# Performance work log

Measured on AMD Instinct MI355X. Metric: run time of the kernel, lower is better.

The kernel has to match this reference:

```python
import jax, jax.numpy as jnp
import numpy as np

HEAD = 32  # HEAD_SIZE
B, T, C = 8, 1024, 768
LAYER_ID, N_LAYER = 2, 12


def wkv7(r, w, k, v, a, b):
    # RWKV7 linear recurrence (matches the custom CUDA 'attn' kernel math):
    #   S = S * exp(-exp(w)) + (S @ a) b^T + v k^T ;  y = S @ r
    Bb, Tt, Cc = r.shape
    H, N = Cc // HEAD, HEAD
    rs = lambda z: jnp.moveaxis(z.reshape(Bb, Tt, H, N), 1, 0)  # [T,B,H,N]
    rT, kT, vT, aT, bT = rs(r), rs(k), rs(v), rs(a), rs(b)
    wT = rs(jnp.exp(-jnp.exp(w)))  # decay in (0,1)
    def step(S, inp):
        rt, wt, kt, vt, at, bt = inp  # each [B,H,N]
        sa = jnp.einsum('bhij,bhj->bhi', S, at)
        S = S * wt[:, :, None, :] + sa[..., None] * bt[:, :, None, :] + vt[..., None] * kt[:, :, None, :]
        return S, jnp.einsum('bhij,bhj->bhi', S, rt)
    S0 = jnp.zeros((Bb, H, N, N), r.dtype)
    _, y = jax.lax.scan(step, S0, (rT, wT, kT, vT, aT, bT))
    return jnp.moveaxis(y, 0, 1).reshape(Bb, Tt, Cc)


def setup_inputs() -> dict:
    key = jax.random.key(0)
    ks = iter(jax.random.split(key, 64))
    def rn(shape, s=0.02):
        return (jax.random.normal(next(ks), shape, jnp.float32) * s)
    def un(shape, lim):
        return jax.random.uniform(next(ks), shape, jnp.float32, -lim, lim)
    H, N = C // HEAD, HEAD
    r10 = 1.0 - LAYER_ID / N_LAYER          # ratio_1_to_almost0
    r01 = LAYER_ID / (N_LAYER - 1)          # ratio_0_to_1
    ddd = (np.arange(C, dtype=np.float64) / C).reshape(1, 1, C)
    f32 = lambda z: jnp.asarray(z, jnp.float32)
    time_maa_x = f32(1.0 - ddd ** (0.6 * r10 ** 0.9))
    time_maa_rg = f32(1.0 - ddd ** (0.2 * r10))
    time_maa_wa = f32(1.0 - ddd ** (0.9 * r10))
    time_maa_k = f32(1.0 - (ddd ** (0.9 * r10) + 0.4 * r01))
    time_maa_v = f32(1.0 - (ddd ** (0.4 * r10) + 0.6 * r01))
    ds = -7.0 + 5.0 * (np.arange(C, dtype=np.float64) / (C - 1)) ** (0.85 + r01 ** 0.5)
    time_decay = f32(ds.reshape(1, 1, C) + 0.5)
    inp = {
        'x': jax.random.normal(next(ks), (B, T, C), jnp.float32),
        'v1': jax.random.normal(next(ks), (B, T, C), jnp.float32),
        'time_maa_x': time_maa_x, 'time_maa_rg': time_maa_rg, 'time_maa_wa': time_maa_wa,
        'time_maa_k': time_maa_k, 'time_maa_v': time_maa_v,
        'time_decay': time_decay,
        'time_faaaa': rn((1, 1, H, N), 0.05),
        'time_aaaaa': rn((1, 1, C), 0.05),
        'time_maa_w1': rn((C, 28 * 4)), 'time_maa_w2': rn((4, 28, C), 0.05),
        'time_decay_w1': rn((C, 64)), 'time_decay_w2': rn((64, C), 0.05),
        'time_aaa_w1': rn((C, 24)), 'time_aaa_w2': rn((24, C), 0.05),
        'time_kkk_w1': rn((C, 24)), 'time_kkk_w2': rn((24, C), 0.05),
        'gate_w1': rn((C, 120)), 'gate_w2': rn((120, C), 0.05),
        'ma_w1': rn((C, 24)), 'ma_w2': rn((24, C), 0.05), 'time_misc_a': rn((1, 1, C), 0.05),
        'mk_w1': rn((C, 24)), 'mk_w2': rn((24, C), 0.05), 'time_misc_k': rn((1, 1, C), 0.05),
        'mv_w1': rn((C, 24)), 'mv_w2': rn((24, C), 0.05), 'time_misc_v': 1.0 + rn((1, 1, C), 0.05),
        'Wr': un((C, C), 0.5 / C ** 0.5), 'Wk': un((C, C), 0.05 / C ** 0.5),
        'Wv': un((C, C), 0.5 / C ** 0.5), 'Wo': rn((C, C), 0.02),
        'ln_w': jnp.ones((C,), jnp.float32), 'ln_b': jnp.zeros((C,), jnp.float32),
    }
    return inp


def reference(x, v1, time_maa_x, time_maa_rg, time_maa_wa, time_maa_k, time_maa_v,
              time_decay, time_faaaa, time_aaaaa, time_maa_w1, time_maa_w2,
              time_decay_w1, time_decay_w2, time_aaa_w1, time_aaa_w2,
              time_kkk_w1, time_kkk_w2, gate_w1, gate_w2, ma_w1, ma_w2, time_misc_a,
              mk_w1, mk_w2, time_misc_k, mv_w1, mv_w2, time_misc_v,
              Wr, Wk, Wv, Wo, ln_w, ln_b):
    Bb, Tt, Cc = x.shape
    H, N = Cc // HEAD, HEAD
    # token shift: xx[t] = x[t-1] - x[t], with x[-1] = 0
    xsh = jnp.concatenate([jnp.zeros_like(x[:, :1]), x[:, :-1]], axis=1)
    xx = xsh - x
    xxx = x + xx * time_maa_x
    tm = jnp.tanh(xxx @ time_maa_w1).reshape(Bb, Tt, 4, -1)      # [B,T,4,28]
    mix = jnp.einsum('btfd,fdc->fbtc', tm, time_maa_w2)          # [4,B,T,C]
    xrg = x + xx * (time_maa_rg + mix[0])
    xwa = x + xx * (time_maa_wa + mix[1])
    xk = x + xx * (time_maa_k + mix[2])
    xv = x + xx * (time_maa_v + mix[3])
    r = xrg @ Wr
    w = -jax.nn.softplus(-(time_decay + jnp.tanh(xwa @ time_decay_w1) @ time_decay_w2)) - 0.5
    k = xk @ Wk
    v = xv @ Wv
    v = v + (v1 - v) * jax.nn.sigmoid(time_misc_v + xv @ mv_w1 @ mv_w2)
    g = jax.nn.sigmoid(xrg @ gate_w1) @ gate_w2
    kk = k + jnp.tanh(xk @ time_kkk_w1) @ time_kkk_w2
    kk4 = kk.reshape(Bb, Tt, H, N)
    nrm = jnp.maximum(jnp.sqrt(jnp.sum(kk4 * kk4, axis=-1, keepdims=True)), 1e-12)
    kk = (kk4 / nrm).reshape(Bb, Tt, Cc)
    a = jax.nn.sigmoid(time_aaaaa + xwa @ time_aaa_w1 @ time_aaa_w2)
    ma = jax.nn.sigmoid(time_misc_a + xwa @ ma_w1 @ ma_w2)
    k = k * ma + k * a * (1.0 - ma)
    mk = jax.nn.sigmoid(time_misc_k + xk @ mk_w1 @ mk_w2)
    k = k * jnp.exp(jnp.minimum(w * mk, 0.0))
    y = wkv7(r, w, k, v, -kk, kk * a)
    # GroupNorm(n_head groups) over each token, eps=6.4e-5
    yg = y.reshape(Bb, Tt, H, N)
    mu = jnp.mean(yg, axis=-1, keepdims=True)
    var = jnp.var(yg, axis=-1, keepdims=True)
    yn = (yg - mu) * jax.lax.rsqrt(var + 6.4e-05)
    yn = yn * ln_w.reshape(H, N) + ln_b.reshape(H, N)
    # per-head bonus term
    bonus = (jnp.sum(r.reshape(Bb, Tt, H, N) * k.reshape(Bb, Tt, H, N) * time_faaaa,
                     axis=-1, keepdims=True) * v.reshape(Bb, Tt, H, N))
    y = yn.reshape(Bb, Tt, Cc) + bonus.reshape(Bb, Tt, Cc)
    out = (y * g) @ Wo
    return (out, v1)
```

## Files before the change

kernel.cpp:

```cpp
#include <hip/hip_runtime.h>
#include <hip/hip_bf16.h>
#include <math.h>

#define Bdim 8
#define Tdim 1024
#define Cdim 768
#define Hdim 24
#define Ndim 32
#define BTdim (Bdim*Tdim)

typedef __attribute__((ext_vector_type(8))) short bf16x8;
typedef __attribute__((ext_vector_type(4))) float f32x4;
typedef __hip_bfloat16 bf16;

__device__ __forceinline__ float sigm(float x){ return 1.f/(1.f+expf(-x)); }
__device__ __forceinline__ float softplusf(float x){ return fmaxf(x,0.f) + log1pf(expf(-fabsf(x))); }
__device__ __forceinline__ float bf2f(bf16 v){ return __bfloat162float(v); }
__device__ __forceinline__ float us2f(unsigned short s){ return __builtin_bit_cast(float, (unsigned)s<<16); }

template<int CTRL>
__device__ __forceinline__ float dpp_add(float x){
  int xi = __builtin_bit_cast(int, x);
  int yi = __builtin_amdgcn_mov_dpp(xi, CTRL, 0xF, 0xF, true);
  return x + __builtin_bit_cast(float, yi);
}
__device__ __forceinline__ float red32(float x){
  x = dpp_add<0xB1>(x);
  x = dpp_add<0x4E>(x);
  x = dpp_add<0x141>(x);
  x = dpp_add<0x140>(x);
  x += __shfl_xor(x, 16);
  return x;
}
__device__ __forceinline__ float red16(float x){
  x = dpp_add<0xB1>(x);
  x = dpp_add<0x4E>(x);
  x = dpp_add<0x141>(x);
  x = dpp_add<0x140>(x);
  return x;
}

#define GLDS16(gp, lp) __builtin_amdgcn_global_load_lds((const __attribute__((address_space(1))) void*)(gp), (__attribute__((address_space(3))) void*)(lp), 16, 0, 0)

__global__ void k1_shift(const float* __restrict__ x, const float* __restrict__ maa_x,
                         bf16* __restrict__ xxx) {
  int idx = blockIdx.x*256 + threadIdx.x;
  if (idx >= BTdim*Cdim) return;
  int c = idx % Cdim; int row = idx / Cdim; int t = row % Tdim;
  float xv = x[idx];
  float xp = (t==0) ? 0.f : x[idx - Cdim];
  xxx[idx] = __float2bfloat16(xv + (xp - xv)*maa_x[c]);
}

__global__ __launch_bounds__(256) void kcp(const float* __restrict__ W0, const float* __restrict__ W1,
    const float* __restrict__ W2, const float* __restrict__ W3,
    bf16* __restrict__ T0, bf16* __restrict__ T1, bf16* __restrict__ T2, bf16* __restrict__ T3,
    const float* __restrict__ dw1, const float* __restrict__ aaa_w1,
    const float* __restrict__ ma_w1, const float* __restrict__ kkk_w1, const float* __restrict__ mk_w1,
    const float* __restrict__ mv_w1, const float* __restrict__ gate_w1, const float* __restrict__ maa_w1,
    const float* __restrict__ dw2, const float* __restrict__ aaa_w2, const float* __restrict__ ma_w2,
    const float* __restrict__ kkk_w2, const float* __restrict__ mk_w2, const float* __restrict__ mv_w2,
    const float* __restrict__ gate_w2,
    bf16* __restrict__ PWwa, bf16* __restrict__ PWk, bf16* __restrict__ PWv,
    bf16* __restrict__ PWrg, bf16* __restrict__ PWmaa,
    bf16* __restrict__ W2wa, bf16* __restrict__ W2k, bf16* __restrict__ W2v, bf16* __restrict__ W2g){
  const int bid = blockIdx.x;
  if (bid < 2304) {
    __shared__ float tile[32][33];
    const int z = bid/576, rem = bid - z*576;
    const int by = (rem/24)*32, bx = (rem%24)*32;
    const float* Wsrc[4] = {W0,W1,W2,W3};
    bf16* Tdst[4] = {T0,T1,T2,T3};
    const float* W = Wsrc[z];
    bf16* T = Tdst[z];
    int tx = threadIdx.x & 31, ty = threadIdx.x >> 5;
    #pragma unroll
    for (int q=0;q<32;q+=8) tile[ty+q][tx] = W[(size_t)(by+ty+q)*Cdim + bx+tx];
    __syncthreads();
    #pragma unroll
    for (int q=0;q<32;q+=8) T[(size_t)(bx+ty+q)*Cdim + by+tx] = __float2bfloat16(tile[tx][ty+q]);
    return;
  }
  int idx = (bid-2304)*256 + threadIdx.x;
  if (idx < 491520) {
    int buf = idx / 98304, rem = idx - buf*98304;
    int n = rem / 768, kk = rem - n*768;
    float val = 0.f;
    bf16* dst;
    switch(buf){
      case 0: dst=PWwa; if(n<64) val=dw1[(size_t)kk*64+n]; else if(n<88) val=aaa_w1[(size_t)kk*24+(n-64)]; else if(n<112) val=ma_w1[(size_t)kk*24+(n-88)]; break;
      case 1: dst=PWk;  if(n<24) val=kkk_w1[(size_t)kk*24+n]; else if(n<48) val=mk_w1[(size_t)kk*24+(n-24)]; break;
      case 2: dst=PWv;  if(n<24) val=mv_w1[(size_t)kk*24+n]; break;
      case 3: dst=PWrg; if(n<120) val=gate_w1[(size_t)kk*120+n]; break;
      default: dst=PWmaa; if(n<112) val=maa_w1[(size_t)kk*112+n]; break;
    }
    dst[rem] = __float2bfloat16(val);
    return;
  }
  int i = idx - 491520;
  if (i < 294912){
    int n=i>>7, q=i&127, seg=n/768, c=n-seg*768;
    float val=0.f;
    if (seg==0){ if(q<64) val=dw2[(size_t)q*768+c]; }
    else if (seg==1){ if(q>=64&&q<88) val=aaa_w2[(size_t)(q-64)*768+c]; }
    else { if(q>=88&&q<112) val=ma_w2[(size_t)(q-88)*768+c]; }
    W2wa[i]=__float2bfloat16(val); return;
  }
  i -= 294912;
  if (i < 98304){
    int n=i>>6, q=i&63, seg=n/768, c=n-seg*768;
    float val=0.f;
    if (seg==0){ if(q<24) val=kkk_w2[(size_t)q*768+c]; }
    else { if(q>=24&&q<48) val=mk_w2[(size_t)(q-24)*768+c]; }
    W2k[i]=__float2bfloat16(val); return;
  }
  i -= 98304;
  if (i < 24576){
    int c=i>>5, q=i&31;
    float val = (q<24) ? mv_w2[(size_t)q*768+c] : 0.f;
    W2v[i]=__float2bfloat16(val); return;
  }
  i -= 24576;
  if (i < 98304){
    int c=i>>7, q=i&127;
    float val = (q<120) ? gate_w2[(size_t)q*768+c] : 0.f;
    W2g[i]=__float2bfloat16(val);
  }
}

__global__ __launch_bounds__(256) void gemm_wo(const bf16* __restrict__ A,
    const bf16* __restrict__ Bt, float* __restrict__ C, int N, int K) {
  const int bid = blockIdx.x;
  const int bm = (bid & 127)*64, bn = (bid >> 7)*128;
  __shared__ unsigned short As[64*32];
  __shared__ unsigned short Bs[128*32];
  const int tid = threadIdx.x, lane = tid&63, w = tid>>6;
  const int wr = w>>1, wc = w&1;
  const int lr = lane&15, kg = lane>>4;
  f32x4 zero = {0.f,0.f,0.f,0.f};
  f32x4 acc[2][4];
  #pragma unroll
  for (int m=0;m<2;m++)
    #pragma unroll
    for (int n=0;n<4;n++) acc[m][n]=zero;
  const size_t rowA = (size_t)(bm + w*16 + (lane>>2))*K + (lane&3)*8;
  const size_t rowB = (size_t)(bn + w*32 + (lane>>2))*K + (lane&3)*8;
  unsigned short* lA = As + w*16*32;
  unsigned short* lB = Bs + w*32*32;
  for (int k0=0; k0<K; k0+=32){
    GLDS16(A + rowA + k0,                 lA);
    GLDS16(Bt + rowB + k0,                lB);
    GLDS16(Bt + rowB + k0 + (size_t)16*K, lB + 512);
    __syncthreads();
    bf16x8 af[2], bfr[4];
    #pragma unroll
    for (int m=0;m<2;m++) af[m]  = *(const bf16x8*)(void*)(As + (wr*32+m*16+lr)*32 + kg*8);
    #pragma unroll
    for (int n=0;n<4;n++) bfr[n] = *(const bf16x8*)(void*)(Bs + (wc*64+n*16+lr)*32 + kg*8);
    #pragma unroll
    for (int m=0;m<2;m++)
      #pragma unroll
      for (int n=0;n<4;n++)
        acc[m][n] = __builtin_amdgcn_mfma_f32_16x16x32_bf16(af[m], bfr[n], acc[m][n], 0,0,0);
    __syncthreads();
  }
  #pragma unroll
  for (int m=0;m<2;m++)
    #pragma unroll
    for (int n=0;n<4;n++){
      size_t r0 = (size_t)(bm + wr*32 + m*16 + kg*4);
      int cc = bn + wc*64 + n*16 + lr;
      #pragma unroll
      for (int q=0;q<4;q++)
        C[(r0+q)*N + cc] = acc[m][n][q];
    }
}

__global__ __launch_bounds__(256) void gemm_tm(const bf16* __restrict__ A,
    const bf16* __restrict__ Bt, float* __restrict__ C, int K) {
  const int bm = blockIdx.x*64;
  __shared__ unsigned short As[64*32];
  __shared__ unsigned short Bs[128*32];
  const int tid = threadIdx.x, lane = tid&63, w = tid>>6;
  const int wr = w>>1, wc = w&1;
  const int lr = lane&15, kg = lane>>4;
  f32x4 zero = {0.f,0.f,0.f,0.f};
  f32x4 acc[2][4];
  #pragma unroll
  for (int m=0;m<2;m++)
    #pragma unroll
    for (int n=0;n<4;n++) acc[m][n]=zero;
  const size_t rowA = (size_t)(bm + w*16 + (lane>>2))*K + (lane&3)*8;
  const size_t rowB = (size_t)(w*32 + (lane>>2))*K + (lane&3)*8;
  unsigned short* lA = As + w*16*32;
  unsigned short* lB = Bs + w*32*32;
  for (int k0=0; k0<K; k0+=32){
    GLDS16(A + rowA + k0,                 lA);
    GLDS16(Bt + rowB + k0,                lB);
    GLDS16(Bt + rowB + k0 + (size_t)16*K, lB + 512);
    __syncthreads();
    bf16x8 af[2], bfr[4];
    #pragma unroll
    for (int m=0;m<2;m++) af[m]  = *(const bf16x8*)(void*)(As + (wr*32+m*16+lr)*32 + kg*8);
    #pragma unroll
    for (int n=0;n<4;n++) bfr[n] = *(const bf16x8*)(void*)(Bs + (wc*64+n*16+lr)*32 + kg*8);
    #pragma unroll
    for (int m=0;m<2;m++)
      #pragma unroll
      for (int n=0;n<4;n++)
        acc[m][n] = __builtin_amdgcn_mfma_f32_16x16x32_bf16(af[m], bfr[n], acc[m][n], 0,0,0);
    __syncthreads();
  }
  #pragma unroll
  for (int m=0;m<2;m++)
    #pragma unroll
    for (int n=0;n<4;n++){
      size_t r0 = (size_t)(bm + wr*32 + m*16 + kg*4);
      int cc = wc*64 + n*16 + lr;
      if (cc < 112){
        #pragma unroll
        for (int q=0;q<4;q++)
          C[(r0+q)*112 + cc] = tanhf(acc[m][n][q]);
      }
    }
}

struct S1P {
  const bf16* A[4];
  const bf16* Bt[4];
  bf16* C[4];
  int Ntrue[4];
  int Nalloc[4];
  int act[4];
};
struct G3 {
  const bf16* A[3];
  const bf16* Bt[3];
  bf16* C[3];
};
__global__ __launch_bounds__(256) void gemm_s1b3(S1P s, G3 g, int K) {
  const int bid = blockIdx.x;
  __shared__ unsigned short As[128*32];
  __shared__ unsigned short Bs[128*32];
  const int tid = threadIdx.x, lane = tid&63, w = tid>>6;
  const int wr = w>>1, wc = w&1;
  const int lr = lane&15, kg = lane>>4;
  int bm, bn, z;
  const bf16 *A, *Bt;
  const bool small = (bid < 256);
  if (small){
    z = bid>>6; bm = (bid&63)*128; bn = 0;
    A = s.A[z]; Bt = s.Bt[z];
  } else {
    int rem = bid-256;
    bn = (rem/192)*128; int t2 = rem%192;
    z = t2/64; bm = (t2%64)*128;
    A = g.A[z]; Bt = g.Bt[z];
  }
  f32x4 zero = {0.f,0.f,0.f,0.f};
  f32x4 acc[4][4];
  #pragma unroll
  for (int m=0;m<4;m++)
    #pragma unroll
    for (int n=0;n<4;n++) acc[m][n]=zero;
  const size_t rowA = (size_t)(bm + w*32 + (lane>>2))*K + (lane&3)*8;
  const size_t rowB = (size_t)(bn + w*32 + (lane>>2))*K + (lane&3)*8;
  unsigned short* lA = As + w*32*32;
  unsigned short* lB = Bs + w*32*32;
  for (int k0=0; k0<K; k0+=32){
    GLDS16(A + rowA + k0,                 lA);
    GLDS16(A + rowA + k0 + (size_t)16*K,  lA + 512);
    GLDS16(Bt + rowB + k0,                lB);
    GLDS16(Bt + rowB + k0 + (size_t)16*K, lB + 512);
    __syncthreads();
    bf16x8 af[4], bfr[4];
    #pragma unroll
    for (int m=0;m<4;m++) af[m]  = *(const bf16x8*)(void*)(As + (wr*64+m*16+lr)*32 + kg*8);
    #pragma unroll
    for (int n=0;n<4;n++) bfr[n] = *(const bf16x8*)(void*)(Bs + (wc*64+n*16+lr)*32 + kg*8);
    #pragma unroll
    for (int m=0;m<4;m++)
      #pragma unroll
      for (int n=0;n<4;n++)
        acc[m][n] = __builtin_amdgcn_mfma_f32_16x16x32_bf16(af[m], bfr[n], acc[m][n], 0,0,0);
    __syncthreads();
  }
  if (small){
    bf16* __restrict__ C = s.C[z];
    const int Ntrue = s.Ntrue[z], Nalloc = s.Nalloc[z], act = s.act[z];
    #pragma unroll
    for (int m=0;m<4;m++)
      #pragma unroll
      for (int n=0;n<4;n++){
        size_t r0 = (size_t)(bm + wr*64 + m*16 + kg*4);
        int cc = wc*64 + n*16 + lr;
        if (cc < Nalloc){
          #pragma unroll
          for (int q=0;q<4;q++){
            float val = acc[m][n][q];
            if      (act==1){ if (cc<64) val = tanhf(val); }
            else if (act==2){ if (cc<24) val = tanhf(val); }
            else if (act==3){ val = sigm(val); }
            if (cc >= Ntrue) val = 0.f;
            C[(r0+q)*Nalloc + cc] = __float2bfloat16(val);
          }
        }
      }
  } else {
    bf16* __restrict__ C = g.C[z];
    #pragma unroll
    for (int m=0;m<4;m++)
      #pragma unroll
      for (int n=0;n<4;n++){
        size_t r0 = (size_t)(bm + wr*64 + m*16 + kg*4);
        int cc = bn + wc*64 + n*16 + lr;
        #pragma unroll
        for (int q=0;q<4;q++)
          C[(r0+q)*Cdim + cc] = __float2bfloat16(acc[m][n][q]);
      }
  }
}

struct Z4 {
  const bf16* A[4];
  const bf16* Bt[4];
  bf16* C[4];
  int N[4];
  int K[4];
};
__global__ __launch_bounds__(256) void gemm_z(Z4 p) {
  const int bid = blockIdx.x;
  const int qs = bid >> 6;
  const int bm = (bid & 63) * 128;
  int z, bnq;
  if (qs < 18){ z=0; bnq=qs; }
  else if (qs < 30){ z=1; bnq=qs-18; }
  else if (qs < 36){ z=2; bnq=qs-30; }
  else { z=3; bnq=qs-36; }
  const int bn = bnq*128;
  const int N = p.N[z], K = p.K[z];
  const bf16* __restrict__ A  = p.A[z];
  const bf16* __restrict__ Bt = p.Bt[z];
  bf16* __restrict__ C = p.C[z];
  __shared__ unsigned short As[128*32];
  __shared__ unsigned short Bs[128*32];
  const int tid = threadIdx.x, lane = tid&63, w = tid>>6;
  const int wr = w>>1, wc = w&1;
  const int lr = lane&15, kg = lane>>4;
  f32x4 zero = {0.f,0.f,0.f,0.f};
  f32x4 acc[4][4];
  #pragma unroll
  for (int m=0;m<4;m++)
    #pragma unroll
    for (int n=0;n<4;n++) acc[m][n]=zero;
  const size_t rowA = (size_t)(bm + w*32 + (lane>>2))*K + (lane&3)*8;
  const size_t rowB = (size_t)(bn + w*32 + (lane>>2))*K + (lane&3)*8;
  unsigned short* lA = As + w*32*32;
  unsigned short* lB = Bs + w*32*32;
  for (int k0=0; k0<K; k0+=32){
    GLDS16(A + rowA + k0,                 lA);
    GLDS16(A + rowA + k0 + (size_t)16*K,  lA + 512);
    GLDS16(Bt + rowB + k0,                lB);
    GLDS16(Bt + rowB + k0 + (size_t)16*K, lB + 512);
    __syncthreads();
    bf16x8 af[4], bfr[4];
    #pragma unroll
    for (int m=0;m<4;m++) af[m]  = *(const bf16x8*)(void*)(As + (wr*64+m*16+lr)*32 + kg*8);
    #pragma unroll
    for (int n=0;n<4;n++) bfr[n] = *(const bf16x8*)(void*)(Bs + (wc*64+n*16+lr)*32 + kg*8);
    #pragma unroll
    for (int m=0;m<4;m++)
      #pragma unroll
      for (int n=0;n<4;n++)
        acc[m][n] = __builtin_amdgcn_mfma_f32_16x16x32_bf16(af[m], bfr[n], acc[m][n], 0,0,0);
    __syncthreads();
  }
  #pragma unroll
  for (int m=0;m<4;m++)
    #pragma unroll
    for (int n=0;n<4;n++){
      size_t r0 = (size_t)(bm + wr*64 + m*16 + kg*4);
      int cc = bn + wc*64 + n*16 + lr;
      #pragma unroll
      for (int q=0;q<4;q++)
        C[(r0+q)*N + cc] = __float2bfloat16(acc[m][n][q]);
    }
}

__global__ __launch_bounds__(256) void k2_mix(const float* __restrict__ x,
    const float* __restrict__ tm, const float* __restrict__ w2,
    const float* __restrict__ mrg, const float* __restrict__ mwa,
    const float* __restrict__ mk_, const float* __restrict__ mv_,
    bf16* __restrict__ xrg, bf16* __restrict__ xwa, bf16* __restrict__ xk, bf16* __restrict__ xv) {
  const int row0 = blockIdx.x*8, tid = threadIdx.x;
  __shared__ float stm[8][112];
  for (int idx=tid; idx<8*112; idx+=256){
    int rr=idx/112, q=idx-rr*112;
    stm[rr][q]=tm[(size_t)(row0+rr)*112+q];
  }
  __syncthreads();
  for (int c=tid;c<Cdim;c+=256){
    float x8[8], d8[8];
    #pragma unroll
    for (int rr=0;rr<8;rr++){
      size_t i=(size_t)(row0+rr)*Cdim+c;
      float xv = x[i];
      float xp = (((row0+rr) & (Tdim-1)) == 0) ? 0.f : x[i - Cdim];
      x8[rr]=xv; d8[rr]=xp - xv;
    }
    float mrgc=mrg[c], mwac=mwa[c], mkc=mk_[c], mvc=mv_[c];
    float m0[8]={},m1[8]={},m2[8]={},m3[8]={};
    #pragma unroll 4
    for (int d=0; d<28; d++){
      float w0=w2[(size_t)(d)*Cdim + c];
      float w1=w2[(size_t)(28+d)*Cdim + c];
      float w2v=w2[(size_t)(56+d)*Cdim + c];
      float w3=w2[(size_t)(84+d)*Cdim + c];
      #pragma unroll
      for (int rr=0;rr<8;rr++){
        m0[rr]+=stm[rr][d]*w0; m1[rr]+=stm[rr][28+d]*w1;
        m2[rr]+=stm[rr][56+d]*w2v; m3[rr]+=stm[rr][84+d]*w3;
      }
    }
    #pragma unroll
    for (int rr=0;rr<8;rr++){
      size_t i=(size_t)(row0+rr)*Cdim+c;
      xrg[i]=__float2bfloat16(x8[rr] + d8[rr]*(mrgc+m0[rr]));
      xwa[i]=__float2bfloat16(x8[rr] + d8[rr]*(mwac+m1[rr]));
      xk[i] =__float2bfloat16(x8[rr] + d8[rr]*(mkc+m2[rr]));
      xv[i] =__float2bfloat16(x8[rr] + d8[rr]*(mvc+m3[rr]));
    }
  }
}

__global__ __launch_bounds__(256) void k5_fuse(
    const bf16* __restrict__ zwa, const bf16* __restrict__ zk, const bf16* __restrict__ zv,
    const bf16* __restrict__ rbf, const bf16* __restrict__ kbf, bf16* __restrict__ vbf,
    const float* __restrict__ td, const float* __restrict__ aaaaa,
    const float* __restrict__ misc_a, const float* __restrict__ misc_k, const float* __restrict__ misc_v,
    const float* __restrict__ v1,
    float* __restrict__ wexp, unsigned short* __restrict__ rkab) {
  const int row = blockIdx.x, tid = threadIdx.x;
  #pragma unroll
  for (int it=0;it<3;it++){
    const int c = tid + it*256;
    const size_t i = (size_t)row*Cdim + c;
    float kraw = bf2f(kbf[i]);
    float v0   = bf2f(vbf[i]);
    float zd = bf2f(zwa[(size_t)row*2304 + c]);
    float za = bf2f(zwa[(size_t)row*2304 + 768 + c]);
    float zma= bf2f(zwa[(size_t)row*2304 + 1536 + c]);
    float zkk= bf2f(zk[(size_t)row*1536 + c]);
    float zmk= bf2f(zk[(size_t)row*1536 + 768 + c]);
    float zmv= bf2f(zv[i]);
    float w = -softplusf(-(td[c]+zd)) - 0.5f;
    wexp[i] = expf(-expf(w));
    float a  = sigm(aaaaa[c]+za);
    float ma = sigm(misc_a[c]+zma);
    float mk = sigm(misc_k[c]+zmk);
    float mv = sigm(misc_v[c]+zmv);
    vbf[i] = __float2bfloat16(v0 + (v1[i]-v0)*mv);
    float kf = kraw*(ma + a*(1.f-ma))*expf(fminf(w*mk,0.f));
    float kk = kraw + zkk;
    float ss = red32(kk*kk);
    float kkn = kk * (1.f/fmaxf(sqrtf(ss),1e-12f));
    unsigned rus = (unsigned)__builtin_bit_cast(unsigned short, rbf[i]);
    unsigned kus = (unsigned)__builtin_bit_cast(unsigned short, __float2bfloat16(kf));
    unsigned aus = (unsigned)__builtin_bit_cast(unsigned short, __float2bfloat16(-kkn));
    unsigned bus = (unsigned)__builtin_bit_cast(unsigned short, __float2bfloat16(kkn*a));
    uint2 pk;
    pk.x = rus | (kus<<16);
    pk.y = aus | (bus<<16);
    *(uint2*)&rkab[((size_t)row*Hdim + (c>>5))*128 + (size_t)(c&31)*4] = pk;
  }
}

__global__ __launch_bounds__(64) void k6_wkv(const unsigned short* __restrict__ rkab,
    const float* __restrict__ wd, const unsigned short* __restrict__ vbf, bf16* __restrict__ y) {
  const int lane = threadIdx.x;
  const int bid = blockIdx.x;
  const int head = bid % (Bdim*Hdim);
  const int rq   = bid / (Bdim*Hdim);
  const int bb = head / Hdim, hh = head - bb*Hdim;
  const int i0 = rq*4 + (lane >> 4);
  const int jh = lane & 15;
  __shared__ __align__(16) unsigned short srk[2][16][128];
  __shared__ __align__(16) float sw[2][16][32];
  __shared__ __align__(16) unsigned short sv[2][16][32];
  const size_t wvbase = (size_t)bb*Tdim*Cdim + (size_t)hh*Ndim;
  float S0=0.f, S1=0.f;

  auto rkrow = [&](size_t t){ return (((size_t)bb*Tdim + t)*Hdim + hh)*128; };
  auto STAGE = [&](int c, int buf){
    const size_t tb = (size_t)c*16;
    #pragma unroll
    for (int i=0;i<4;i++)
      GLDS16(rkab + rkrow(tb + i*4 + (lane>>4)) + (size_t)(lane&15)*8, &srk[buf][i*4][0]);
    GLDS16(wd + wvbase + (tb +     (lane>>3))*Cdim + (lane&7)*4, &sw[buf][0][0]);
    GLDS16(wd + wvbase + (tb + 8 + (lane>>3))*Cdim + (lane&7)*4, &sw[buf][8][0]);
    GLDS16(vbf + wvbase + (tb + (lane>>2))*Cdim + (lane&3)*8, &sv[buf][0][0]);
  };

  uint4 nq; float2 nw; unsigned short nv;
  auto LOADT = [&](int buf, int t){
    nq = *(const uint4*)&srk[buf][t][jh*8];
    nw = *(const float2*)&sw[buf][t][jh*2];
    nv = sv[buf][t][i0];
  };

  STAGE(0, 0);
  asm volatile("s_waitcnt vmcnt(0)" ::: "memory");
  LOADT(0, 0);
  int buf = 0;
  const int NCH = Tdim/16;
  for (int c=0; c<NCH; ++c){
    if (c+1 < NCH) STAGE(c+1, buf^1);
    const size_t yb = wvbase + (size_t)c*16*Cdim;
    #pragma unroll
    for (int t=0; t<16; t++){
      const uint4 q = nq;
      const float2 cw = nw;
      const unsigned short cv = nv;
      if (t < 15) {
        LOADT(buf, t+1);
      } else if (c+1 < NCH) {
        asm volatile("s_waitcnt vmcnt(0)" ::: "memory");
        LOADT(buf^1, 0);
      }
      float r0 = __builtin_bit_cast(float, q.x<<16);
      float k0 = __builtin_bit_cast(float, q.x & 0xFFFF0000u);
      float a0 = __builtin_bit_cast(float, q.y<<16);
      float b0 = __builtin_bit_cast(float, q.y & 0xFFFF0000u);
      float r1 = __builtin_bit_cast(float, q.z<<16);
      float k1 = __builtin_bit_cast(float, q.z & 0xFFFF0000u);
      float a1 = __builtin_bit_cast(float, q.w<<16);
      float b1 = __builtin_bit_cast(float, q.w & 0xFFFF0000u);
      const float vl = us2f(cv);
      float sa = S0*a0 + S1*a1;
      sa = red16(sa);
      S0 = S0*cw.x + (sa*b0 + vl*k0);
      S1 = S1*cw.y + (sa*b1 + vl*k1);
      float yv = S0*r0 + S1*r1;
      yv = red16(yv);
      if (jh == 0) y[yb + (size_t)t*Cdim + i0] = __float2bfloat16(yv);
    }
    buf ^= 1;
  }
}

__global__ __launch_bounds__(256) void k7_post(const bf16* __restrict__ y,
    const unsigned short* __restrict__ rkab, const bf16* __restrict__ v,
    const bf16* __restrict__ g, const float* __restrict__ faaaa,
    const float* __restrict__ lnw, const float* __restrict__ lnb,
    bf16* __restrict__ ygate,
    const float4* __restrict__ v1c, float4* __restrict__ outc) {
  const int row = blockIdx.x, tid = threadIdx.x;
  if (tid < 192) outc[(size_t)row*192 + tid] = v1c[(size_t)row*192 + tid];
  #pragma unroll
  for (int it=0; it<3; it++){
    const int c = tid + it*256;
    const size_t i = (size_t)row*Cdim + c;
    float yv = bf2f(y[i]);
    unsigned rk = *(const unsigned*)&rkab[((size_t)row*Hdim + (c>>5))*128 + (size_t)(c&31)*4];
    float rf = __builtin_bit_cast(float, rk<<16);
    float kf = __builtin_bit_cast(float, rk & 0xFFFF0000u);
    float bon = rf*kf*faaaa[c];
    float s  = red32(yv);
    float ss = red32(yv*yv);
    float bn = red32(bon);
    float mu = s*(1.f/Ndim);
    float var = ss*(1.f/Ndim) - mu*mu;
    float rs = rsqrtf(var + 6.4e-5f);
    float yn = (yv-mu)*rs*lnw[c]+lnb[c];
    ygate[i]=__float2bfloat16((yn + bn*bf2f(v[i]))*bf2f(g[i]));
  }
}

extern "C" void kernel_launch(void* const* d_in, const int* in_sizes, int n_in,
                              void* d_out, int out_size, void* d_ws, size_t ws_size,
                              hipStream_t stream) {
  const float* x      = (const float*)d_in[0];
  const float* v1     = (const float*)d_in[1];
  const float* maa_x  = (const float*)d_in[2];
  const float* maa_rg = (const float*)d_in[3];
  const float* maa_wa = (const float*)d_in[4];
  const float* maa_k  = (const float*)d_in[5];
  const float* maa_v  = (const float*)d_in[6];
  const float* time_decay = (const float*)d_in[7];
  const float* faaaa  = (const float*)d_in[8];
  const float* aaaaa  = (const float*)d_in[9];
  const float* maa_w1 = (const float*)d_in[10];
  const float* maa_w2 = (const float*)d_in[11];
  const float* dw1    = (const float*)d_in[12];
  const float* dw2    = (const float*)d_in[13];
  const float* aaa_w1 = (const float*)d_in[14];
  const float* aaa_w2 = (const float*)d_in[15];
  const float* kkk_w1 = (const float*)d_in[16];
  const float* kkk_w2 = (const float*)d_in[17];
  const float* gate_w1= (const float*)d_in[18];
  const float* gate_w2= (const float*)d_in[19];
  const float* ma_w1  = (const float*)d_in[20];
  const float* ma_w2  = (const float*)d_in[21];
  const float* misc_a = (const float*)d_in[22];
  const float* mk_w1  = (const float*)d_in[23];
  const float* mk_w2  = (const float*)d_in[24];
  const float* misc_k = (const float*)d_in[25];
  const float* mv_w1  = (const float*)d_in[26];
  const float* mv_w2  = (const float*)d_in[27];
  const float* misc_v = (const float*)d_in[28];
  const float* Wr     = (const float*)d_in[29];
  const float* Wk     = (const float*)d_in[30];
  const float* Wv     = (const float*)d_in[31];
  const float* Wo     = (const float*)d_in[32];
  const float* lnw    = (const float*)d_in[33];
  const float* lnb    = (const float*)d_in[34];
  float* out = (float*)d_out;

  float* ws = (float*)d_ws;
  const size_t BTC = (size_t)BTdim*Cdim;
  const size_t HB  = BTC/2;
  float* wexp  = ws;
  bf16* kb_bf  = (bf16*)(ws + 2*HB);
  bf16* ybuf_bf= (bf16*)(ws + 2*HB);
  bf16* vb_bf  = (bf16*)(ws + 3*HB);
  bf16* xrg_bf = (bf16*)(ws + 4*HB);
  bf16* xwa_bf = xrg_bf + BTC;
  bf16* zwa_bf = (bf16*)(ws + 4*HB);
  bf16* xk_bf  = (bf16*)(ws + 7*HB);
  bf16* xv_bf  = xk_bf + BTC;
  bf16* zk_bf  = (bf16*)(ws + 7*HB);
  bf16* xxx_bf = (bf16*)(ws + 9*HB);
  bf16* zv_bf  = (bf16*)(ws + 9*HB);
  float* tm    = ws + 10*HB;
  bf16* zg_bf  = (bf16*)(ws + 10*HB);
  bf16* hwa_bf = (bf16*)(ws + 11*HB);
  bf16* hk_bf  = hwa_bf + (size_t)BTdim*128;
  bf16* hv_bf  = hk_bf  + (size_t)BTdim*64;
  bf16* hrg_bf = hv_bf  + (size_t)BTdim*32;
  unsigned short* rkab = (unsigned short*)(ws + 12*HB);
  bf16* rb_bf  = (bf16*)(ws + 16*HB);
  bf16* yg_bf  = (bf16*)(ws + 17*HB);
  bf16* Wbase  = (bf16*)(ws + 18*HB);
  bf16* WtR = Wbase;
  bf16* WtK = WtR + 589824;
  bf16* WtV = WtK + 589824;
  bf16* WtO = WtV + 589824;
  bf16* PWwa = WtO + 589824;
  bf16* PWk  = PWwa + 98304;
  bf16* PWv  = PWk  + 98304;
  bf16* PWrg = PWv  + 98304;
  bf16* PWmaa= PWrg + 98304;
  bf16* W2wa = PWmaa + 98304;
  bf16* W2k  = W2wa + 294912;
  bf16* W2v  = W2k  + 98304;
  bf16* W2g  = W2v  + 24576;

  dim3 blk(256);
  k1_shift<<<dim3((BTdim*Cdim+255)/256), blk, 0, stream>>>(x, maa_x, xxx_bf);
  kcp<<<dim3(2304+3936), blk, 0, stream>>>(Wr,Wk,Wv,Wo, WtR,WtK,WtV,WtO,
                                           dw1,aaa_w1,ma_w1,kkk_w1,mk_w1,mv_w1,gate_w1,maa_w1,
                                           dw2,aaa_w2,ma_w2,kkk_w2,mk_w2,mv_w2,gate_w2,
                                           PWwa,PWk,PWv,PWrg,PWmaa, W2wa,W2k,W2v,W2g);
  gemm_tm<<<dim3(128), blk, 0, stream>>>(xxx_bf, PWmaa, tm, Cdim);
  k2_mix<<<dim3(BTdim/8), blk, 0, stream>>>(x, tm, maa_w2, maa_rg, maa_wa, maa_k, maa_v,
                                            xrg_bf, xwa_bf, xk_bf, xv_bf);
  {
    S1P s{};
    s.A[0]=xwa_bf; s.Bt[0]=PWwa; s.C[0]=hwa_bf; s.Ntrue[0]=112; s.Nalloc[0]=128; s.act[0]=1;
    s.A[1]=xk_bf;  s.Bt[1]=PWk;  s.C[1]=hk_bf;  s.Ntrue[1]=48;  s.Nalloc[1]=64;  s.act[1]=2;
    s.A[2]=xv_bf;  s.Bt[2]=PWv;  s.C[2]=hv_bf;  s.Ntrue[2]=24;  s.Nalloc[2]=32;  s.act[2]=0;
    s.A[3]=xrg_bf; s.Bt[3]=PWrg; s.C[3]=hrg_bf; s.Ntrue[3]=120; s.Nalloc[3]=128; s.act[3]=3;
    G3 g{};
    g.A[0]=xrg_bf; g.Bt[0]=WtR; g.C[0]=rb_bf;
    g.A[1]=xk_bf;  g.Bt[1]=WtK; g.C[1]=kb_bf;
    g.A[2]=xv_bf;  g.Bt[2]=WtV; g.C[2]=vb_bf;
    gemm_s1b3<<<dim3(256 + 3*384), blk, 0, stream>>>(s, g, Cdim);
  }
  {
    Z4 p{};
    p.A[0]=hwa_bf; p.Bt[0]=W2wa; p.C[0]=zwa_bf; p.N[0]=2304; p.K[0]=128;
    p.A[1]=hk_bf;  p.Bt[1]=W2k;  p.C[1]=zk_bf;  p.N[1]=1536; p.K[1]=64;
    p.A[2]=hv_bf;  p.Bt[2]=W2v;  p.C[2]=zv_bf;  p.N[2]=768;  p.K[2]=32;
    p.A[3]=hrg_bf; p.Bt[3]=W2g;  p.C[3]=zg_bf;  p.N[3]=768;  p.K[3]=128;
    gemm_z<<<dim3(42*64), blk, 0, stream>>>(p);
  }
  k5_fuse<<<dim3(BTdim), blk, 0, stream>>>(zwa_bf, zk_bf, zv_bf, rb_bf, kb_bf, vb_bf,
      time_decay, aaaaa, misc_a, misc_k, misc_v, v1, wexp, rkab);
  k6_wkv<<<dim3(Bdim*Hdim*8), dim3(64), 0, stream>>>(rkab, wexp,
      (const unsigned short*)vb_bf, ybuf_bf);
  k7_post<<<dim3(BTdim), blk, 0, stream>>>(ybuf_bf, rkab, vb_bf, zg_bf, faaaa, lnw, lnb, yg_bf,
                                           (const float4*)v1, (float4*)(out + BTC));
  gemm_wo<<<dim3(768), blk, 0, stream>>>(yg_bf, WtO, out, Cdim, Cdim);
}
```

Before: 493.0 us.

## Break the sa reduction dependency in the WKV recurrence with a lookahead algebraic split

Computes next step's S·a as P + sa·(b·a') + v·(k·a'). P comes from the pre-update state times decay times the next a, so the cross-lane reduction no longer sits directly on the per-step serial chain. LDS operand loads are now double-buffered two timesteps ahead to supply the next a values. This adds two extra DPP reductions per step and changes float summation order.

```diff
diff --git a/kernel.cpp b/kernel.cpp
--- a/kernel.cpp
+++ b/kernel.cpp
@@ -475,6 +475,7 @@
   }
 }
 
+struct TRq { uint4 q; float2 w; unsigned short v; };
 __global__ __launch_bounds__(64) void k6_wkv(const unsigned short* __restrict__ rkab,
     const float* __restrict__ wd, const unsigned short* __restrict__ vbf, bf16* __restrict__ y) {
   const int lane = threadIdx.x;
@@ -489,6 +490,8 @@
   __shared__ __align__(16) unsigned short sv[2][16][32];
   const size_t wvbase = (size_t)bb*Tdim*Cdim + (size_t)hh*Ndim;
   float S0=0.f, S1=0.f;
+  float saP=0.f, vlP=0.f;
+  float P=0.f, BA=0.f, KA=0.f;
 
   auto rkrow = [&](size_t t){ return (((size_t)bb*Tdim + t)*Hdim + hh)*128; };
   auto STAGE = [&](int c, int buf){
@@ -500,17 +503,17 @@
     GLDS16(wd + wvbase + (tb + 8 + (lane>>3))*Cdim + (lane&7)*4, &sw[buf][8][0]);
     GLDS16(vbf + wvbase + (tb + (lane>>2))*Cdim + (lane&3)*8, &sv[buf][0][0]);
   };
-
-  uint4 nq; float2 nw; unsigned short nv;
-  auto LOADT = [&](int buf, int t){
-    nq = *(const uint4*)&srk[buf][t][jh*8];
-    nw = *(const float2*)&sw[buf][t][jh*2];
-    nv = sv[buf][t][i0];
+  auto LOADT = [&](TRq& d, int buf, int t){
+    d.q = *(const uint4*)&srk[buf][t][jh*8];
+    d.w = *(const float2*)&sw[buf][t][jh*2];
+    d.v = sv[buf][t][i0];
   };
 
   STAGE(0, 0);
   asm volatile("s_waitcnt vmcnt(0)" ::: "memory");
-  LOADT(0, 0);
+  TRq pA, pB;
+  LOADT(pA, 0, 0);
+  LOADT(pB, 0, 1);
   int buf = 0;
   const int NCH = Tdim/16;
   for (int c=0; c<NCH; ++c){
@@ -518,31 +521,38 @@
     const size_t yb = wvbase + (size_t)c*16*Cdim;
     #pragma unroll
     for (int t=0; t<16; t++){
-      const uint4 q = nq;
-      const float2 cw = nw;
-      const unsigned short cv = nv;
-      if (t < 15) {
-        LOADT(buf, t+1);
+      TRq& cur = (t&1) ? pB : pA;
+      TRq& nxt = (t&1) ? pA : pB;
+      const uint4 q = cur.q;
+      const float2 cw = cur.w;
+      const unsigned short cv = cur.v;
+      const float na0 = __builtin_bit_cast(float, nxt.q.y<<16);
+      const float na1 = __builtin_bit_cast(float, nxt.q.w<<16);
+      const int tt = t+2;
+      if (tt < 16) {
+        LOADT(cur, buf, tt);
       } else if (c+1 < NCH) {
-        asm volatile("s_waitcnt vmcnt(0)" ::: "memory");
-        LOADT(buf^1, 0);
+        if (tt == 16) asm volatile("s_waitcnt vmcnt(0)" ::: "memory");
+        LOADT(cur, buf^1, tt-16);
       }
-      float r0 = __builtin_bit_cast(float, q.x<<16);
-      float k0 = __builtin_bit_cast(float, q.x & 0xFFFF0000u);
-      float a0 = __builtin_bit_cast(float, q.y<<16);
-      float b0 = __builtin_bit_cast(float, q.y & 0xFFFF0000u);
-      float r1 = __builtin_bit_cast(float, q.z<<16);
-      float k1 = __builtin_bit_cast(float, q.z & 0xFFFF0000u);
-      float a1 = __builtin_bit_cast(float, q.w<<16);
-      float b1 = __builtin_bit_cast(float, q.w & 0xFFFF0000u);
+      const float r0 = __builtin_bit_cast(float, q.x<<16);
+      const float k0 = __builtin_bit_cast(float, q.x & 0xFFFF0000u);
+      const float b0 = __builtin_bit_cast(float, q.y & 0xFFFF0000u);
+      const float r1 = __builtin_bit_cast(float, q.z<<16);
+      const float k1 = __builtin_bit_cast(float, q.z & 0xFFFF0000u);
+      const float b1 = __builtin_bit_cast(float, q.w & 0xFFFF0000u);
       const float vl = us2f(cv);
-      float sa = S0*a0 + S1*a1;
-      sa = red16(sa);
+      const float sa = P + saP*BA + vlP*KA;
+      const float pa = S0*(cw.x*na0) + S1*(cw.y*na1);
       S0 = S0*cw.x + (sa*b0 + vl*k0);
       S1 = S1*cw.y + (sa*b1 + vl*k1);
       float yv = S0*r0 + S1*r1;
       yv = red16(yv);
       if (jh == 0) y[yb + (size_t)t*Cdim + i0] = __float2bfloat16(yv);
+      P  = red16(pa);
+      BA = red16(b0*na0 + b1*na1);
+      KA = red16(k0*na0 + k1*na1);
+      saP = sa; vlP = vl;
     }
     buf ^= 1;
   }
```

Result: slower. 554.0 us (+12.4%).
